# Optimization experiments

Measured on AMD Instinct MI355X. Metric: run time of the kernel, lower is better.

The kernel has to match this reference:

```python
import jax, jax.numpy as jnp
import numpy as np

WH, WW = 8, 8
N_TOK = WH * WW
NUM_HEADS = 4
DIM = 128
B_WIN = 4096  # num_windows * B
NW = 64       # windows per image (for mask)


def _make_rel_tables():
    # relative coords table (1, 2*Wh-1, 2*Ww-1, 2), log-spaced as in SwinV2
    ch = np.arange(-(WH - 1), WH, dtype=np.float32)
    cw = np.arange(-(WW - 1), WW, dtype=np.float32)
    t = np.stack(np.meshgrid(ch, cw, indexing='ij'), axis=-1)[None]  # (1,15,15,2)
    t[..., 0] /= (WH - 1)
    t[..., 1] /= (WW - 1)
    t *= 8
    t = np.sign(t) * np.log2(np.abs(t) + 1.0) / np.log2(8)
    # relative position index (N, N)
    coords = np.stack(np.meshgrid(np.arange(WH), np.arange(WW), indexing='ij'))
    cf = coords.reshape(2, -1)
    rel = cf[:, :, None] - cf[:, None, :]
    rel = rel.transpose(1, 2, 0).copy()
    rel[:, :, 0] += WH - 1
    rel[:, :, 1] += WW - 1
    rel[:, :, 0] *= 2 * WW - 1
    idx = rel.sum(-1).astype(np.int32)
    return jnp.asarray(t), jnp.asarray(idx)


def setup_inputs() -> dict:
    key = jax.random.key(0)
    ks = jax.random.split(key, 8)
    table, idx = _make_rel_tables()
    return {
        'x': jax.random.normal(ks[0], (B_WIN, N_TOK, DIM), jnp.float32),
        'context': jax.random.normal(ks[1], (B_WIN, N_TOK, DIM), jnp.float32),
        'mask': jnp.zeros((NW, N_TOK, N_TOK), jnp.float32),
        'q_w': jax.random.normal(ks[2], (DIM, DIM), jnp.float32) * 0.02,
        'q_b': jnp.zeros((DIM,), jnp.float32),
        'kv_w': jax.random.normal(ks[3], (2 * DIM, DIM), jnp.float32) * 0.02,
        'v_b': jnp.zeros((DIM,), jnp.float32),
        'logit_scale': jnp.full((NUM_HEADS, 1, 1), np.log(10.0), jnp.float32),
        'cpb_w1': jax.random.normal(ks[4], (512, 2), jnp.float32) * 0.02,
        'cpb_b1': jnp.zeros((512,), jnp.float32),
        'cpb_w2': jax.random.normal(ks[5], (NUM_HEADS, 512), jnp.float32) * 0.02,
        'proj_w': jax.random.normal(ks[6], (DIM, DIM), jnp.float32) * 0.02,
        'proj_b': jnp.zeros((DIM,), jnp.float32),
        'rel_coords_table': table,
        'rel_pos_index': idx,
    }


def _l2norm(t, eps=1e-12):
    return t / jnp.maximum(jnp.linalg.norm(t, axis=-1, keepdims=True), eps)


def reference(x, context, mask, q_w, q_b, kv_w, v_b, logit_scale,
              cpb_w1, cpb_b1, cpb_w2, proj_w, proj_b,
              rel_coords_table, rel_pos_index):
    B_, N, C = x.shape
    H = NUM_HEADS
    hd = C // H
    # projections (kv bias = [zeros_like(v_b); v_b])
    q = x @ q_w.T + q_b
    kv_bias = jnp.concatenate([jnp.zeros_like(v_b), v_b])
    kv = context @ kv_w.T + kv_bias
    q = q.reshape(B_, N, H, hd).transpose(0, 2, 1, 3)          # (B_,H,N,hd)
    kv = kv.reshape(B_, N, 2, H, hd).transpose(2, 0, 3, 1, 4)  # (2,B_,H,N,hd)
    k, v = kv[0], kv[1]
    # cosine attention with clamped learned scale
    attn = jnp.einsum('bhnd,bhmd->bhnm', _l2norm(q), _l2norm(k))
    scale = jnp.exp(jnp.minimum(logit_scale, np.log(1.0 / 0.01)))  # (H,1,1)
    attn = attn * scale[None]
    # CPB-MLP relative position bias
    hidd = jax.nn.relu(rel_coords_table @ cpb_w1.T + cpb_b1)   # (1,15,15,512)
    table = (hidd @ cpb_w2.T).reshape(-1, H)                   # ((2Wh-1)(2Ww-1), H)
    bias = table[rel_pos_index.reshape(-1)].reshape(N, N, H)
    bias = 16.0 * jax.nn.sigmoid(bias.transpose(2, 0, 1))      # (H,N,N)
    attn = attn + bias[None]
    # shift mask
    nW = mask.shape[0]
    attn = attn.reshape(B_ // nW, nW, H, N, N) + mask[None, :, None]
    attn = attn.reshape(B_, H, N, N)
    attn = jax.nn.softmax(attn, axis=-1)
    out = jnp.einsum('bhnm,bhmd->bhnd', attn, v)
    out = out.transpose(0, 2, 1, 3).reshape(B_, N, C)
    return out @ proj_w.T + proj_b
```

## Files before the change

### kernel.cpp

```cpp
#include <hip/hip_runtime.h>
#include <hip/hip_bf16.h>

#define NT 64
#define DIM 128

typedef __attribute__((ext_vector_type(8))) short short8;
typedef __attribute__((ext_vector_type(4))) short short4v;
typedef __attribute__((ext_vector_type(8))) __bf16 bf16x8;
typedef __attribute__((ext_vector_type(4))) float floatx4;
typedef __attribute__((ext_vector_type(4))) unsigned uintx4;

#define MFMA(a,b,c) __builtin_amdgcn_mfma_f32_16x16x32_bf16(a,b,c,0,0,0)
#define SWZ(idx, row) ((idx) ^ (((row)&7)<<3))

__device__ __forceinline__ short bfbits(float f) {
  return __builtin_bit_cast(short, (__bf16)f);
}
__device__ __forceinline__ unsigned pk2(float lo, float hi) {
  return (unsigned)(unsigned short)__builtin_bit_cast(unsigned short, (__bf16)lo)
       | ((unsigned)(unsigned short)__builtin_bit_cast(unsigned short, (__bf16)hi) << 16);
}
__device__ __forceinline__ bf16x8 frag_bf(const short* __restrict__ p) {
  return __builtin_bit_cast(bf16x8, *(const short8*)p);
}
// ... 26 lines not shown
        a1 += h * w2[512 + j];
        a2 += h * w2[1024 + j];
        a3 += h * w2[1536 + j];
      }
      logits[t][0]=a0; logits[t][1]=a1; logits[t][2]=a2; logits[t][3]=a3;
    }
    __syncthreads();
    for (int f = t; f < 16384; f += 256) {
      int i    = f & 3;
      int lane = (f >> 2) & 63;
      int qt   = (f >> 8) & 3;
      int mk   = (f >> 10) & 3;
      int h    = f >> 12;
      int q = qt*16 + (lane & 15);
      int k = mk*16 + ((lane >> 4) & 3)*4 + i;
      int p = idx[q*64 + k];
      float v = logits[p][h];
      bias_packed[f] = 16.f / (1.f + __expf(-v));
    }
  } else {
    int gidx = (blockIdx.x - 1) * 4096 + t * 16;
    const float* src; int off;
    if (gidx < 16384)      { src = q_w;    off = gidx; }
    else if (gidx < 49152) { src = kv_w;   off = gidx - 16384; }
    else                   { src = proj_w; off = gidx - 49152; }
    const float4* s = (const float4*)(src + off);
    short* dst = wbf + gidx;
#pragma unroll
    for (int i = 0; i < 2; ++i)
      *(short8*)(dst + i*8) = pack8(s[2*i], s[2*i+1]);
  }
}

__global__ __launch_bounds__(512, 6)
void swin_ctx_attn_kernel(const float* __restrict__ x, const float* __restrict__ ctx,
                          const float* __restrict__ mask,
                          const short* __restrict__ wq, const float* __restrict__ q_b,
                          const short* __restrict__ wkv, const float* __restrict__ v_b,
                          const float* __restrict__ logit_scale,
                          const short* __restrict__ wproj, const float* __restrict__ proj_b,
                          const float* __restrict__ bias_p,
                          float* __restrict__ out) {
  __shared__ short lds[24576] __attribute__((aligned(16)));
  const int tid  = threadIdx.x;
  const int lane = tid & 63;
  const int wv   = tid >> 6;
  const int h    = wv >> 1;
  const int s    = wv & 1;
  const int b    = blockIdx.x;
  const int lr   = lane & 15;
  const int lg   = lane >> 4;

  short* xb   = lds;
  short* cb   = lds + 8192;
  short* kn   = lds + 16384;
  short* vT   = xb;
  short* outp = cb;
  short* knh  = kn + h*2048;

  const float* xw = x   + (size_t)b*(NT*DIM);
  const float* cw = ctx + (size_t)b*(NT*DIM);

  {
    const int sr = tid >> 3, sc0 = (tid & 7) * 16;
    const float4* xs = (const float4*)(xw + sr*DIM + sc0);
    const float4* cs = (const float4*)(cw + sr*DIM + sc0);
    float4 xr[4], cr[4];
#pragma unroll
    for (int i = 0; i < 4; ++i) xr[i] = xs[i];
#pragma unroll
    for (int i = 0; i < 4; ++i) cr[i] = cs[i];
#pragma unroll
    for (int i = 0; i < 2; ++i)
      *(short8*)(xb + SWZ(sr*128 + sc0 + i*8, sr)) = pack8(xr[2*i], xr[2*i+1]);
#pragma unroll
    for (int i = 0; i < 2; ++i)
      *(short8*)(cb + SWZ(sr*128 + sc0 + i*8, sr)) = pack8(cr[2*i], cr[2*i+1]);
  }
  __syncthreads();

  const int sA = ((lane & 16) << 1) | (lane & 15);
  const int sB = sA + 16;
  const unsigned selp = (lane & 32) ? 0x07060302u : 0x05040100u;

  bf16x8 qB[2];
  float scl = __expf(fminf(logit_scale[h], 4.605170185988091f));
  {
    floatx4 aq[2][2] = {};
    for (int ks = 0; ks < 4; ++ks) {
      bf16x8 xf[2], wf[2];
#pragma unroll
      for (int n = 0; n < 2; ++n) {
        int tok = (2*s + n)*16 + lr;
        xf[n] = frag_bf(xb + SWZ(tok*128 + ks*32 + lg*8, tok));
      }
#pragma unroll
      for (int mc = 0; mc < 2; ++mc)
        wf[mc] = frag_bf(wq + (h*32 + mc*16 + lr)*DIM + ks*32 + lg*8);
#pragma unroll
      for (int mc = 0; mc < 2; ++mc)
#pragma unroll
        for (int n = 0; n < 2; ++n)
          aq[mc][n] = MFMA(wf[mc], xf[n], aq[mc][n]);
    }
    floatx4 qb4[2];
#pragma unroll
    for (int mc = 0; mc < 2; ++mc)
      qb4[mc] = *(const floatx4*)(q_b + h*32 + mc*16 + lg*4);
#pragma unroll
    for (int n = 0; n < 2; ++n) {
      float ss = 0.f;
#pragma unroll
      for (int mc = 0; mc < 2; ++mc)
#pragma unroll
        for (int i = 0; i < 4; ++i) {
          aq[mc][n][i] += qb4[mc][i];
          ss += aq[mc][n][i]*aq[mc][n][i];
        }
      ss += __shfl_xor(ss, 16, 64);
      ss += __shfl_xor(ss, 32, 64);
      float sc = scl / fmaxf(sqrtf(ss), 1e-12f);
#pragma unroll
      for (int mc = 0; mc < 2; ++mc)
#pragma unroll
        for (int i = 0; i < 4; ++i) aq[mc][n][i] *= sc;
      unsigned pq[4], w[8];
#pragma unroll
      for (int i = 0; i < 4; ++i) pq[i] = pk2(aq[0][n][i], aq[1][n][i]);
#pragma unroll
      for (int j = 0; j < 8; ++j) w[j] = __shfl(pq[j & 3], (j < 4) ? sA : sB, 64);
      uintx4 u;
#pragma unroll
      for (int t = 0; t < 4; ++t) u[t] = __builtin_amdgcn_perm(w[2*t+1], w[2*t], selp);
      qB[n] = __builtin_bit_cast(bf16x8, u);
    }
  }

  {
    floatx4 ak[2][2] = {};
    for (int ks = 0; ks < 4; ++ks) {
      bf16x8 cf[2], wkf[2];
#pragma unroll
      for (int r = 0; r < 2; ++r) {
        int tok = (2*s + r)*16 + lr;
        cf[r] = frag_bf(cb + SWZ(tok*128 + ks*32 + lg*8, tok));
      }
#pragma unroll
      for (int mc = 0; mc < 2; ++mc)
        wkf[mc] = frag_bf(wkv + (h*32 + mc*16 + lr)*DIM + ks*32 + lg*8);
#pragma unroll
      for (int mc = 0; mc < 2; ++mc)
#pragma unroll
        for (int n = 0; n < 2; ++n)
          ak[mc][n] = MFMA(wkf[mc], cf[n], ak[mc][n]);
    }
#pragma unroll
    for (int n = 0; n < 2; ++n) {
      float ss = 0.f;
#pragma unroll
      for (int mc = 0; mc < 2; ++mc)
#pragma unroll
        for (int i = 0; i < 4; ++i) ss += ak[mc][n][i]*ak[mc][n][i];
      ss += __shfl_xor(ss, 16, 64);
      ss += __shfl_xor(ss, 32, 64);
      float sc = 1.0f / fmaxf(sqrtf(ss), 1e-12f);
#pragma unroll
      for (int mc = 0; mc < 2; ++mc)
#pragma unroll
        for (int i = 0; i < 4; ++i) ak[mc][n][i] *= sc;
    }
#pragma unroll
    for (int mc = 0; mc < 2; ++mc)
#pragma unroll
      for (int n = 0; n < 2; ++n) {
        int tok = (2*s + n)*16 + lr;
        short4v t4;
#pragma unroll
        for (int i = 0; i < 4; ++i) t4[i] = bfbits(ak[mc][n][i]);
        *(short4v*)(knh + SWZ(tok*32 + mc*16 + lg*4, tok)) = t4;
      }
  }
  __syncthreads();

  {
    floatx4 av[2][2] = {};
    for (int ks = 0; ks < 4; ++ks) {
      bf16x8 cf[2], wvf[2];
#pragma unroll
      for (int r = 0; r < 2; ++r) {
        int tok = (2*s + r)*16 + lr;
        cf[r] = frag_bf(cb + SWZ(tok*128 + ks*32 + lg*8, tok));
      }
#pragma unroll
      for (int mc = 0; mc < 2; ++mc)
        wvf[mc] = frag_bf(wkv + (DIM + h*32 + mc*16 + lr)*DIM + ks*32 + lg*8);
#pragma unroll
      for (int mc = 0; mc < 2; ++mc)
#pragma unroll
        for (int n = 0; n < 2; ++n)
          av[mc][n] = MFMA(cf[mc], wvf[n], av[mc][n]);
    }
    float vb0 = v_b[h*32 + lr], vb1 = v_b[h*32 + 16 + lr];
#pragma unroll
    for (int m = 0; m < 2; ++m)
#pragma unroll
      for (int n = 0; n < 2; ++n) {
        int chG = h*32 + n*16 + lr;
        float vb = n ? vb1 : vb0;
        short4v t4;
#pragma unroll
        for (int i = 0; i < 4; ++i) t4[i] = bfbits(av[m][n][i] + vb);
        *(short4v*)(vT + SWZ(chG*64 + s*32 + m*16 + lg*4, chG)) = t4;
      }
  }
  __syncthreads();

  floatx4 st[4][2] = {};
#pragma unroll
  for (int mk = 0; mk < 4; ++mk) {
    int tok = mk*16 + lr;
    bf16x8 kf = frag_bf(knh + SWZ(tok*32 + lg*8, tok));
#pragma unroll
    for (int n = 0; n < 2; ++n)
      st[mk][n] = MFMA(kf, qB[n], st[mk][n]);
  }

  float rinv[2];
  {
    int wimg = b & 63;
#pragma unroll
    for (int n = 0; n < 2; ++n) {
      int qcol = (2*s + n)*16 + lr;
#pragma unroll
      for (int mk = 0; mk < 4; ++mk) {
        floatx4 b4 = ((const floatx4*)bias_p)[((h*4 + mk)*4 + (2*s + n))*64 + lane];
        floatx4 m4 = *(const floatx4*)(mask + ((size_t)wimg*64 + qcol)*64 + mk*16 + lg*4);
#pragma unroll
        for (int i = 0; i < 4; ++i) st[mk][n][i] += b4[i] + m4[i];
      }
      float mx = st[0][n][0];
#pragma unroll
      for (int mk = 0; mk < 4; ++mk)
#pragma unroll
        for (int i = 0; i < 4; ++i) mx = fmaxf(mx, st[mk][n][i]);
      mx = fmaxf(mx, __shfl_xor(mx, 16, 64));
      mx = fmaxf(mx, __shfl_xor(mx, 32, 64));
      float sum = 0.f;
#pragma unroll
      for (int mk = 0; mk < 4; ++mk)
#pragma unroll
        for (int i = 0; i < 4; ++i) {
          st[mk][n][i] = __expf(st[mk][n][i] - mx);
          sum += st[mk][n][i];
        }
      sum += __shfl_xor(sum, 16, 64);
      sum += __shfl_xor(sum, 32, 64);
      rinv[n] = 1.0f / sum;
    }
  }

  bf16x8 pB[2][2];
#pragma unroll
  for (int kk = 0; kk < 2; ++kk)
#pragma unroll
    for (int n = 0; n < 2; ++n) {
      unsigned pp[4], w[8];
#pragma unroll
      for (int i = 0; i < 4; ++i) pp[i] = pk2(st[2*kk][n][i], st[2*kk+1][n][i]);
#pragma unroll
      for (int j = 0; j < 8; ++j) w[j] = __shfl(pp[j & 3], (j < 4) ? sA : sB, 64);
      uintx4 u;
#pragma unroll
      for (int t = 0; t < 4; ++t) u[t] = __builtin_amdgcn_perm(w[2*t+1], w[2*t], selp);
      pB[kk][n] = __builtin_bit_cast(bf16x8, u);
    }
  floatx4 ot[2][2] = {};
#pragma unroll
  for (int kk = 0; kk < 2; ++kk) {
    bf16x8 vf[2];
#pragma unroll
    for (int mo = 0; mo < 2; ++mo) {
      int chG = h*32 + mo*16 + lr;
      vf[mo] = frag_bf(vT + SWZ(chG*64 + kk*32 + lg*8, chG));
    }
#pragma unroll
    for (int mo = 0; mo < 2; ++mo)
#pragma unroll
      for (int n = 0; n < 2; ++n)
        ot[mo][n] = MFMA(vf[mo], pB[kk][n], ot[mo][n]);
  }

#pragma unroll
  for (int mo = 0; mo < 2; ++mo)
#pragma unroll
    for (int n = 0; n < 2; ++n) {
      int tok = (2*s + n)*16 + lr;
      short4v t4;
#pragma unroll
      for (int i = 0; i < 4; ++i) t4[i] = bfbits(ot[mo][n][i] * rinv[n]);
      *(short4v*)(outp + SWZ(tok*128 + h*32 + mo*16 + lg*4, tok)) = t4;
    }
  __syncthreads();

  {
    floatx4 ap[2][2] = {};
    for (int ks = 0; ks < 4; ++ks) {
      bf16x8 of[2], wpf[2];
#pragma unroll
      for (int m = 0; m < 2; ++m) {
        int tok = s*32 + m*16 + lr;
        of[m] = frag_bf(outp + SWZ(tok*128 + ks*32 + lg*8, tok));
      }
#pragma unroll
      for (int n = 0; n < 2; ++n)
        wpf[n] = frag_bf(wproj + (h*32 + n*16 + lr)*DIM + ks*32 + lg*8);
#pragma unroll
      for (int m = 0; m < 2; ++m)
#pragma unroll
        for (int n = 0; n < 2; ++n)
          ap[m][n] = MFMA(of[m], wpf[n], ap[m][n]);
    }
    float pb0 = proj_b[h*32 + lr], pb1 = proj_b[h*32 + 16 + lr];
    float* op = out + (size_t)b * (NT*DIM);
#pragma unroll
    for (int m = 0; m < 2; ++m)
#pragma unroll
      for (int n = 0; n < 2; ++n) {
        float pb = n ? pb1 : pb0;
#pragma unroll
        for (int i = 0; i < 4; ++i)
          op[(s*32 + m*16 + lg*4 + i)*DIM + h*32 + n*16 + lr] = ap[m][n][i] + pb;
      }
  }
}

extern "C" void kernel_launch(void* const* d_in, const int* in_sizes, int n_in,
                              void* d_out, int out_size, void* d_ws, size_t ws_size,
                              hipStream_t stream) {
  const float* x     = (const float*)d_in[0];
  const float* ctx   = (const float*)d_in[1];
  const float* mask  = (const float*)d_in[2];
  const float* q_w   = (const float*)d_in[3];
  const float* q_b   = (const float*)d_in[4];
  const float* kv_w  = (const float*)d_in[5];
  const float* v_b   = (const float*)d_in[6];
  const float* ls    = (const float*)d_in[7];
  const float* w1    = (const float*)d_in[8];
  const float* b1    = (const float*)d_in[9];
  const float* w2    = (const float*)d_in[10];
  const float* pw    = (const float*)d_in[11];
  const float* pb    = (const float*)d_in[12];
  const float* table = (const float*)d_in[13];
  const int*   idx   = (const int*)d_in[14];

  float* bias_p = (float*)d_ws;
  short* wbf    = (short*)((char*)d_ws + 65536);
  short* wq     = wbf;
  short* wkv    = wbf + 16384;
  short* wproj  = wbf + 49152;
  int B = in_sizes[0] / (NT * DIM);

  prep_kernel<<<17, 256, 0, stream>>>(table, w1, b1, w2, idx, q_w, kv_w, pw,
                                      bias_p, wbf);
  swin_ctx_attn_kernel<<<B, 512, 0, stream>>>(x, ctx, mask, wq, q_b, wkv, v_b,
                                              ls, wproj, pb, bias_p, (float*)d_out);
}
```

Before: 272.5 us.

## Process two windows per block and prefetch the next window's inputs during compute

Each block now handles two consecutive windows. The second window's x is loaded into registers during the first window's prologue, and its context is loaded while the output projection runs. The idea is to hide global load latency behind MFMA work and to halve the number of blocks launched. In exchange the launch bound drops from 6 to 4 blocks per CU, which raises register pressure and adds extra barriers. The grid also assumes an even window count.

```diff
diff --git a/kernel.cpp b/kernel.cpp
--- a/kernel.cpp
+++ b/kernel.cpp
@@ -82,7 +82,7 @@
   }
 }
 
-__global__ __launch_bounds__(512, 6)
+__global__ __launch_bounds__(512, 4)
 void swin_ctx_attn_kernel(const float* __restrict__ x, const float* __restrict__ ctx,
                           const float* __restrict__ mask,
                           const short* __restrict__ wq, const float* __restrict__ q_b,
@@ -97,7 +97,6 @@
   const int wv   = tid >> 6;
   const int h    = wv >> 1;
   const int s    = wv & 1;
-  const int b    = blockIdx.x;
   const int lr   = lane & 15;
   const int lg   = lane >> 4;
 
@@ -108,280 +107,305 @@
   short* outp = cb;
   short* knh  = kn + h*2048;
 
-  const float* xw = x   + (size_t)b*(NT*DIM);
-  const float* cw = ctx + (size_t)b*(NT*DIM);
-
-  {
-    const int sr = tid >> 3, sc0 = (tid & 7) * 16;
-    const float4* xs = (const float4*)(xw + sr*DIM + sc0);
-    const float4* cs = (const float4*)(cw + sr*DIM + sc0);
-    float4 xr[4], cr[4];
-#pragma unroll
-    for (int i = 0; i < 4; ++i) xr[i] = xs[i];
-#pragma unroll
-    for (int i = 0; i < 4; ++i) cr[i] = cs[i];
-#pragma unroll
-    for (int i = 0; i < 2; ++i)
-      *(short8*)(xb + SWZ(sr*128 + sc0 + i*8, sr)) = pack8(xr[2*i], xr[2*i+1]);
-#pragma unroll
-    for (int i = 0; i < 2; ++i)
-      *(short8*)(cb + SWZ(sr*128 + sc0 + i*8, sr)) = pack8(cr[2*i], cr[2*i+1]);
-  }
-  __syncthreads();
+  const int sr  = tid >> 3;
+  const int sc0 = (tid & 7) * 16;
+  const int b0  = blockIdx.x * 2;
 
   const int sA = ((lane & 16) << 1) | (lane & 15);
   const int sB = sA + 16;
   const unsigned selp = (lane & 32) ? 0x07060302u : 0x05040100u;
-
-  bf16x8 qB[2];
-  float scl = __expf(fminf(logit_scale[h], 4.605170185988091f));
+  const float scl = __expf(fminf(logit_scale[h], 4.605170185988091f));
+
+  float4 xr1[4];
   {
-    floatx4 aq[2][2] = {};
-    for (int ks = 0; ks < 4; ++ks) {
-      bf16x8 xf[2], wf[2];
+    const float4* xs = (const float4*)(x   + (size_t)b0*(NT*DIM) + sr*DIM + sc0);
+    const float4* cs = (const float4*)(ctx + (size_t)b0*(NT*DIM) + sr*DIM + sc0);
+    float4 xr[4], cr[4];
+#pragma unroll
+    for (int i = 0; i < 4; ++i) xr[i] = xs[i];
+#pragma unroll
+    for (int i = 0; i < 4; ++i) cr[i] = cs[i];
+    *(short8*)(xb + SWZ(sr*128 + sc0,     sr)) = pack8(xr[0], xr[1]);
+    *(short8*)(xb + SWZ(sr*128 + sc0 + 8, sr)) = pack8(xr[2], xr[3]);
+    *(short8*)(cb + SWZ(sr*128 + sc0,     sr)) = pack8(cr[0], cr[1]);
+    *(short8*)(cb + SWZ(sr*128 + sc0 + 8, sr)) = pack8(cr[2], cr[3]);
+    const float4* xs1 = (const float4*)(x + (size_t)(b0+1)*(NT*DIM) + sr*DIM + sc0);
+#pragma unroll
+    for (int i = 0; i < 4; ++i) xr1[i] = xs1[i];
+    __builtin_amdgcn_sched_barrier(0);
+  }
+  __syncthreads();
+
+  auto window = [&](int b, bool pre) {
+    bf16x8 qB[2];
+    {
+      floatx4 aq[2][2] = {};
+      for (int ks = 0; ks < 4; ++ks) {
+        bf16x8 xf[2], wf[2];
+#pragma unroll
+        for (int n = 0; n < 2; ++n) {
+          int tok = (2*s + n)*16 + lr;
+          xf[n] = frag_bf(xb + SWZ(tok*128 + ks*32 + lg*8, tok));
+        }
+#pragma unroll
+        for (int mc = 0; mc < 2; ++mc)
+          wf[mc] = frag_bf(wq + (h*32 + mc*16 + lr)*DIM + ks*32 + lg*8);
+#pragma unroll
+        for (int mc = 0; mc < 2; ++mc)
+#pragma unroll
+          for (int n = 0; n < 2; ++n)
+            aq[mc][n] = MFMA(wf[mc], xf[n], aq[mc][n]);
+      }
+      floatx4 qb4[2];
+#pragma unroll
+      for (int mc = 0; mc < 2; ++mc)
+        qb4[mc] = *(const floatx4*)(q_b + h*32 + mc*16 + lg*4);
 #pragma unroll
       for (int n = 0; n < 2; ++n) {
-        int tok = (2*s + n)*16 + lr;
-        xf[n] = frag_bf(xb + SWZ(tok*128 + ks*32 + lg*8, tok));
+        float ss = 0.f;
+#pragma unroll
+        for (int mc = 0; mc < 2; ++mc)
+#pragma unroll
+          for (int i = 0; i < 4; ++i) {
+            aq[mc][n][i] += qb4[mc][i];
+            ss += aq[mc][n][i]*aq[mc][n][i];
+          }
+        ss += __shfl_xor(ss, 16, 64);
+        ss += __shfl_xor(ss, 32, 64);
+        float sc = scl / fmaxf(sqrtf(ss), 1e-12f);
+#pragma unroll
+        for (int mc = 0; mc < 2; ++mc)
+#pragma unroll
+          for (int i = 0; i < 4; ++i) aq[mc][n][i] *= sc;
+        unsigned pq[4], w[8];
+#pragma unroll
+        for (int i = 0; i < 4; ++i) pq[i] = pk2(aq[0][n][i], aq[1][n][i]);
+#pragma unroll
+        for (int j = 0; j < 8; ++j) w[j] = __shfl(pq[j & 3], (j < 4) ? sA : sB, 64);
+        uintx4 u;
+#pragma unroll
+        for (int t = 0; t < 4; ++t) u[t] = __builtin_amdgcn_perm(w[2*t+1], w[2*t], selp);
+        qB[n] = __builtin_bit_cast(bf16x8, u);
+      }
+    }
+
+    {
+      floatx4 ak[2][2] = {};
+      for (int ks = 0; ks < 4; ++ks) {
+        bf16x8 cf[2], wkf[2];
+#pragma unroll
+        for (int r = 0; r < 2; ++r) {
+          int tok = (2*s + r)*16 + lr;
+          cf[r] = frag_bf(cb + SWZ(tok*128 + ks*32 + lg*8, tok));
+        }
+#pragma unroll
+        for (int mc = 0; mc < 2; ++mc)
+          wkf[mc] = frag_bf(wkv + (h*32 + mc*16 + lr)*DIM + ks*32 + lg*8);
+#pragma unroll
+        for (int mc = 0; mc < 2; ++mc)
+#pragma unroll
+          for (int n = 0; n < 2; ++n)
+            ak[mc][n] = MFMA(wkf[mc], cf[n], ak[mc][n]);
+      }
+#pragma unroll
+      for (int n = 0; n < 2; ++n) {
+        float ss = 0.f;
+#pragma unroll
+        for (int mc = 0; mc < 2; ++mc)
+#pragma unroll
+          for (int i = 0; i < 4; ++i) ss += ak[mc][n][i]*ak[mc][n][i];
+        ss += __shfl_xor(ss, 16, 64);
+        ss += __shfl_xor(ss, 32, 64);
+        float sc = 1.0f / fmaxf(sqrtf(ss), 1e-12f);
+#pragma unroll
+        for (int mc = 0; mc < 2; ++mc)
+#pragma unroll
+          for (int i = 0; i < 4; ++i) ak[mc][n][i] *= sc;
       }
 #pragma unroll
       for (int mc = 0; mc < 2; ++mc)
-        wf[mc] = frag_bf(wq + (h*32 + mc*16 + lr)*DIM + ks*32 + lg*8);
-#pragma unroll
-      for (int mc = 0; mc < 2; ++mc)
+#pragma unroll
+        for (int n = 0; n < 2; ++n) {
+          int tok = (2*s + n)*16 + lr;
+          short4v t4;
+#pragma unroll
+          for (int i = 0; i < 4; ++i) t4[i] = bfbits(ak[mc][n][i]);
+          *(short4v*)(knh + SWZ(tok*32 + mc*16 + lg*4, tok)) = t4;
+        }
+    }
+    __syncthreads();
+
+    {
+      floatx4 av[2][2] = {};
+      for (int ks = 0; ks < 4; ++ks) {
+        bf16x8 cf[2], wvf[2];
+#pragma unroll
+        for (int r = 0; r < 2; ++r) {
+          int tok = (2*s + r)*16 + lr;
+          cf[r] = frag_bf(cb + SWZ(tok*128 + ks*32 + lg*8, tok));
+        }
+#pragma unroll
+        for (int mc = 0; mc < 2; ++mc)
+          wvf[mc] = frag_bf(wkv + (DIM + h*32 + mc*16 + lr)*DIM + ks*32 + lg*8);
+#pragma unroll
+        for (int mc = 0; mc < 2; ++mc)
+#pragma unroll
+          for (int n = 0; n < 2; ++n)
+            av[mc][n] = MFMA(cf[mc], wvf[n], av[mc][n]);
+      }
+      float vb0 = v_b[h*32 + lr], vb1 = v_b[h*32 + 16 + lr];
+#pragma unroll
+      for (int m = 0; m < 2; ++m)
+#pragma unroll
+        for (int n = 0; n < 2; ++n) {
+          int chG = h*32 + n*16 + lr;
+          float vb = n ? vb1 : vb0;
+          short4v t4;
+#pragma unroll
+          for (int i = 0; i < 4; ++i) t4[i] = bfbits(av[m][n][i] + vb);
+          *(short4v*)(vT + SWZ(chG*64 + s*32 + m*16 + lg*4, chG)) = t4;
+        }
+    }
+    __syncthreads();
+
+    floatx4 st[4][2] = {};
+#pragma unroll
+    for (int mk = 0; mk < 4; ++mk) {
+      int tok = mk*16 + lr;
+      bf16x8 kf = frag_bf(knh + SWZ(tok*32 + lg*8, tok));
+#pragma unroll
+      for (int n = 0; n < 2; ++n)
+        st[mk][n] = MFMA(kf, qB[n], st[mk][n]);
+    }
+
+    float rinv[2];
+    {
+      int wimg = b & 63;
+#pragma unroll
+      for (int n = 0; n < 2; ++n) {
+        int qcol = (2*s + n)*16 + lr;
+#pragma unroll
+        for (int mk = 0; mk < 4; ++mk) {
+          floatx4 b4 = ((const floatx4*)bias_p)[((h*4 + mk)*4 + (2*s + n))*64 + lane];
+          floatx4 m4 = *(const floatx4*)(mask + ((size_t)wimg*64 + qcol)*64 + mk*16 + lg*4);
+#pragma unroll
+          for (int i = 0; i < 4; ++i) st[mk][n][i] += b4[i] + m4[i];
+        }
+        float mx = st[0][n][0];
+#pragma unroll
+        for (int mk = 0; mk < 4; ++mk)
+#pragma unroll
+          for (int i = 0; i < 4; ++i) mx = fmaxf(mx, st[mk][n][i]);
+        mx = fmaxf(mx, __shfl_xor(mx, 16, 64));
+        mx = fmaxf(mx, __shfl_xor(mx, 32, 64));
+        float sum = 0.f;
+#pragma unroll
+        for (int mk = 0; mk < 4; ++mk)
+#pragma unroll
+          for (int i = 0; i < 4; ++i) {
+            st[mk][n][i] = __expf(st[mk][n][i] - mx);
+            sum += st[mk][n][i];
+          }
+        sum += __shfl_xor(sum, 16, 64);
+        sum += __shfl_xor(sum, 32, 64);
+        rinv[n] = 1.0f / sum;
+      }
+    }
+
+    bf16x8 pB[2][2];
+#pragma unroll
+    for (int kk = 0; kk < 2; ++kk)
+#pragma unroll
+      for (int n = 0; n < 2; ++n) {
+        unsigned pp[4], w[8];
+#pragma unroll
+        for (int i = 0; i < 4; ++i) pp[i] = pk2(st[2*kk][n][i], st[2*kk+1][n][i]);
+#pragma unroll
+        for (int j = 0; j < 8; ++j) w[j] = __shfl(pp[j & 3], (j < 4) ? sA : sB, 64);
+        uintx4 u;
+#pragma unroll
+        for (int t = 0; t < 4; ++t) u[t] = __builtin_amdgcn_perm(w[2*t+1], w[2*t], selp);
+        pB[kk][n] = __builtin_bit_cast(bf16x8, u);
+      }
+    floatx4 ot[2][2] = {};
+#pragma unroll
+    for (int kk = 0; kk < 2; ++kk) {
+      bf16x8 vf[2];
+#pragma unroll
+      for (int mo = 0; mo < 2; ++mo) {
+        int chG = h*32 + mo*16 + lr;
+        vf[mo] = frag_bf(vT + SWZ(chG*64 + kk*32 + lg*8, chG));
+      }
+#pragma unroll
+      for (int mo = 0; mo < 2; ++mo)
 #pragma unroll
         for (int n = 0; n < 2; ++n)
-          aq[mc][n] = MFMA(wf[mc], xf[n], aq[mc][n]);
-    }
-    floatx4 qb4[2];
-#pragma unroll
-    for (int mc = 0; mc < 2; ++mc)
-      qb4[mc] = *(const floatx4*)(q_b + h*32 + mc*16 + lg*4);
-#pragma unroll
-    for (int n = 0; n < 2; ++n) {
-      float ss = 0.f;
-#pragma unroll
-      for (int mc = 0; mc < 2; ++mc)
-#pragma unroll
-        for (int i = 0; i < 4; ++i) {
-          aq[mc][n][i] += qb4[mc][i];
-          ss += aq[mc][n][i]*aq[mc][n][i];
-        }
-      ss += __shfl_xor(ss, 16, 64);
-      ss += __shfl_xor(ss, 32, 64);
-      float sc = scl / fmaxf(sqrtf(ss), 1e-12f);
-#pragma unroll
-      for (int mc = 0; mc < 2; ++mc)
-#pragma unroll
-        for (int i = 0; i < 4; ++i) aq[mc][n][i] *= sc;
-      unsigned pq[4], w[8];
-#pragma unroll
-      for (int i = 0; i < 4; ++i) pq[i] = pk2(aq[0][n][i], aq[1][n][i]);
-#pragma unroll
-      for (int j = 0; j < 8; ++j) w[j] = __shfl(pq[j & 3], (j < 4) ? sA : sB, 64);
-      uintx4 u;
-#pragma unroll
-      for (int t = 0; t < 4; ++t) u[t] = __builtin_amdgcn_perm(w[2*t+1], w[2*t], selp);
-      qB[n] = __builtin_bit_cast(bf16x8, u);
-    }
-  }
-
-  {
-    floatx4 ak[2][2] = {};
-    for (int ks = 0; ks < 4; ++ks) {
-      bf16x8 cf[2], wkf[2];
-#pragma unroll
-      for (int r = 0; r < 2; ++r) {
-        int tok = (2*s + r)*16 + lr;
-        cf[r] = frag_bf(cb + SWZ(tok*128 + ks*32 + lg*8, tok));
-      }
-#pragma unroll
-      for (int mc = 0; mc < 2; ++mc)
-        wkf[mc] = frag_bf(wkv + (h*32 + mc*16 + lr)*DIM + ks*32 + lg*8);
-#pragma unroll
-      for (int mc = 0; mc < 2; ++mc)
-#pragma unroll
-        for (int n = 0; n < 2; ++n)
-          ak[mc][n] = MFMA(wkf[mc], cf[n], ak[mc][n]);
-    }
-#pragma unroll
-    for (int n = 0; n < 2; ++n) {
-      float ss = 0.f;
-#pragma unroll
-      for (int mc = 0; mc < 2; ++mc)
-#pragma unroll
-        for (int i = 0; i < 4; ++i) ss += ak[mc][n][i]*ak[mc][n][i];
-      ss += __shfl_xor(ss, 16, 64);
-      ss += __shfl_xor(ss, 32, 64);
-      float sc = 1.0f / fmaxf(sqrtf(ss), 1e-12f);
-#pragma unroll
-      for (int mc = 0; mc < 2; ++mc)
-#pragma unroll
-        for (int i = 0; i < 4; ++i) ak[mc][n][i] *= sc;
-    }
-#pragma unroll
-    for (int mc = 0; mc < 2; ++mc)
+          ot[mo][n] = MFMA(vf[mo], pB[kk][n], ot[mo][n]);
+    }
+
+#pragma unroll
+    for (int mo = 0; mo < 2; ++mo)
 #pragma unroll
       for (int n = 0; n < 2; ++n) {
         int tok = (2*s + n)*16 + lr;
         short4v t4;
 #pragma unroll
-        for (int i = 0; i < 4; ++i) t4[i] = bfbits(ak[mc][n][i]);
-        *(short4v*)(knh + SWZ(tok*32 + mc*16 + lg*4, tok)) = t4;
-      }
-  }
+        for (int i = 0; i < 4; ++i) t4[i] = bfbits(ot[mo][n][i] * rinv[n]);
+        *(short4v*)(outp + SWZ(tok*128 + h*32 + mo*16 + lg*4, tok)) = t4;
+      }
+    __syncthreads();
+
+    float4 cr1[4];
+    if (pre) {
+      const float4* cs1 = (const float4*)(ctx + (size_t)(b+1)*(NT*DIM) + sr*DIM + sc0);
+#pragma unroll
+      for (int i = 0; i < 4; ++i) cr1[i] = cs1[i];
+      *(short8*)(xb + SWZ(sr*128 + sc0,     sr)) = pack8(xr1[0], xr1[1]);
+      *(short8*)(xb + SWZ(sr*128 + sc0 + 8, sr)) = pack8(xr1[2], xr1[3]);
+      __builtin_amdgcn_sched_barrier(0);
+    }
+
+    {
+      floatx4 ap[2][2] = {};
+      for (int ks = 0; ks < 4; ++ks) {
+        bf16x8 of[2], wpf[2];
+#pragma unroll
+        for (int m = 0; m < 2; ++m) {
+          int tok = s*32 + m*16 + lr;
+          of[m] = frag_bf(outp + SWZ(tok*128 + ks*32 + lg*8, tok));
+        }
+#pragma unroll
+        for (int n = 0; n < 2; ++n)
+          wpf[n] = frag_bf(wproj + (h*32 + n*16 + lr)*DIM + ks*32 + lg*8);
+#pragma unroll
+        for (int m = 0; m < 2; ++m)
+#pragma unroll
+          for (int n = 0; n < 2; ++n)
+            ap[m][n] = MFMA(of[m], wpf[n], ap[m][n]);
+      }
+      float pb0 = proj_b[h*32 + lr], pb1 = proj_b[h*32 + 16 + lr];
+      float* op = out + (size_t)b * (NT*DIM);
+#pragma unroll
+      for (int m = 0; m < 2; ++m)
+#pragma unroll
+        for (int n = 0; n < 2; ++n) {
+          float pb = n ? pb1 : pb0;
+#pragma unroll
+          for (int i = 0; i < 4; ++i)
+            op[(s*32 + m*16 + lg*4 + i)*DIM + h*32 + n*16 + lr] = ap[m][n][i] + pb;
+        }
+    }
+
+    if (pre) {
+      __syncthreads();
+      *(short8*)(cb + SWZ(sr*128 + sc0,     sr)) = pack8(cr1[0], cr1[1]);
+      *(short8*)(cb + SWZ(sr*128 + sc0 + 8, sr)) = pack8(cr1[2], cr1[3]);
+    }
+  };
+
+  window(b0, true);
   __syncthreads();
-
-  {
-    floatx4 av[2][2] = {};
-    for (int ks = 0; ks < 4; ++ks) {
-      bf16x8 cf[2], wvf[2];
-#pragma unroll
-      for (int r = 0; r < 2; ++r) {
-        int tok = (2*s + r)*16 + lr;
-        cf[r] = frag_bf(cb + SWZ(tok*128 + ks*32 + lg*8, tok));
-      }
-#pragma unroll
-      for (int mc = 0; mc < 2; ++mc)
-        wvf[mc] = frag_bf(wkv + (DIM + h*32 + mc*16 + lr)*DIM + ks*32 + lg*8);
-#pragma unroll
-      for (int mc = 0; mc < 2; ++mc)
-#pragma unroll
-        for (int n = 0; n < 2; ++n)
-          av[mc][n] = MFMA(cf[mc], wvf[n], av[mc][n]);
-    }
-    float vb0 = v_b[h*32 + lr], vb1 = v_b[h*32 + 16 + lr];
-#pragma unroll
-    for (int m = 0; m < 2; ++m)
-#pragma unroll
-      for (int n = 0; n < 2; ++n) {
-        int chG = h*32 + n*16 + lr;
-        float vb = n ? vb1 : vb0;
-        short4v t4;
-#pragma unroll
-        for (int i = 0; i < 4; ++i) t4[i] = bfbits(av[m][n][i] + vb);
-        *(short4v*)(vT + SWZ(chG*64 + s*32 + m*16 + lg*4, chG)) = t4;
-      }
-  }
-  __syncthreads();
-
-  floatx4 st[4][2] = {};
-#pragma unroll
-  for (int mk = 0; mk < 4; ++mk) {
-    int tok = mk*16 + lr;
-    bf16x8 kf = frag_bf(knh + SWZ(tok*32 + lg*8, tok));
-#pragma unroll
-    for (int n = 0; n < 2; ++n)
-      st[mk][n] = MFMA(kf, qB[n], st[mk][n]);
-  }
-
-  float rinv[2];
-  {
-    int wimg = b & 63;
-#pragma unroll
-    for (int n = 0; n < 2; ++n) {
-      int qcol = (2*s + n)*16 + lr;
-#pragma unroll
-      for (int mk = 0; mk < 4; ++mk) {
-        floatx4 b4 = ((const floatx4*)bias_p)[((h*4 + mk)*4 + (2*s + n))*64 + lane];
-        floatx4 m4 = *(const floatx4*)(mask + ((size_t)wimg*64 + qcol)*64 + mk*16 + lg*4);
-#pragma unroll
-        for (int i = 0; i < 4; ++i) st[mk][n][i] += b4[i] + m4[i];
-      }
-      float mx = st[0][n][0];
-#pragma unroll
-      for (int mk = 0; mk < 4; ++mk)
-#pragma unroll
-        for (int i = 0; i < 4; ++i) mx = fmaxf(mx, st[mk][n][i]);
-      mx = fmaxf(mx, __shfl_xor(mx, 16, 64));
-      mx = fmaxf(mx, __shfl_xor(mx, 32, 64));
-      float sum = 0.f;
-#pragma unroll
-      for (int mk = 0; mk < 4; ++mk)
-#pragma unroll
-        for (int i = 0; i < 4; ++i) {
-          st[mk][n][i] = __expf(st[mk][n][i] - mx);
-          sum += st[mk][n][i];
-        }
-      sum += __shfl_xor(sum, 16, 64);
-      sum += __shfl_xor(sum, 32, 64);
-      rinv[n] = 1.0f / sum;
-    }
-  }
-
-  bf16x8 pB[2][2];
-#pragma unroll
-  for (int kk = 0; kk < 2; ++kk)
-#pragma unroll
-    for (int n = 0; n < 2; ++n) {
-      unsigned pp[4], w[8];
-#pragma unroll
-      for (int i = 0; i < 4; ++i) pp[i] = pk2(st[2*kk][n][i], st[2*kk+1][n][i]);
-#pragma unroll
-      for (int j = 0; j < 8; ++j) w[j] = __shfl(pp[j & 3], (j < 4) ? sA : sB, 64);
-      uintx4 u;
-#pragma unroll
-      for (int t = 0; t < 4; ++t) u[t] = __builtin_amdgcn_perm(w[2*t+1], w[2*t], selp);
-      pB[kk][n] = __builtin_bit_cast(bf16x8, u);
-    }
-  floatx4 ot[2][2] = {};
-#pragma unroll
-  for (int kk = 0; kk < 2; ++kk) {
-    bf16x8 vf[2];
-#pragma unroll
-    for (int mo = 0; mo < 2; ++mo) {
-      int chG = h*32 + mo*16 + lr;
-      vf[mo] = frag_bf(vT + SWZ(chG*64 + kk*32 + lg*8, chG));
-    }
-#pragma unroll
-    for (int mo = 0; mo < 2; ++mo)
-#pragma unroll
-      for (int n = 0; n < 2; ++n)
-        ot[mo][n] = MFMA(vf[mo], pB[kk][n], ot[mo][n]);
-  }
-
-#pragma unroll
-  for (int mo = 0; mo < 2; ++mo)
-#pragma unroll
-    for (int n = 0; n < 2; ++n) {
-      int tok = (2*s + n)*16 + lr;
-      short4v t4;
-#pragma unroll
-      for (int i = 0; i < 4; ++i) t4[i] = bfbits(ot[mo][n][i] * rinv[n]);
-      *(short4v*)(outp + SWZ(tok*128 + h*32 + mo*16 + lg*4, tok)) = t4;
-    }
-  __syncthreads();
-
-  {
-    floatx4 ap[2][2] = {};
-    for (int ks = 0; ks < 4; ++ks) {
-      bf16x8 of[2], wpf[2];
-#pragma unroll
-      for (int m = 0; m < 2; ++m) {
-        int tok = s*32 + m*16 + lr;
-        of[m] = frag_bf(outp + SWZ(tok*128 + ks*32 + lg*8, tok));
-      }
-#pragma unroll
-      for (int n = 0; n < 2; ++n)
-        wpf[n] = frag_bf(wproj + (h*32 + n*16 + lr)*DIM + ks*32 + lg*8);
-#pragma unroll
-      for (int m = 0; m < 2; ++m)
-#pragma unroll
-        for (int n = 0; n < 2; ++n)
-          ap[m][n] = MFMA(of[m], wpf[n], ap[m][n]);
-    }
-    float pb0 = proj_b[h*32 + lr], pb1 = proj_b[h*32 + 16 + lr];
-    float* op = out + (size_t)b * (NT*DIM);
-#pragma unroll
-    for (int m = 0; m < 2; ++m)
-#pragma unroll
-      for (int n = 0; n < 2; ++n) {
-        float pb = n ? pb1 : pb0;
-#pragma unroll
-        for (int i = 0; i < 4; ++i)
-          op[(s*32 + m*16 + lg*4 + i)*DIM + h*32 + n*16 + lr] = ap[m][n][i] + pb;
-      }
-  }
+  window(b0 + 1, false);
 }
 
 extern "C" void kernel_launch(void* const* d_in, const int* in_sizes, int n_in,
@@ -412,6 +436,6 @@
 
   prep_kernel<<<17, 256, 0, stream>>>(table, w1, b1, w2, idx, q_w, kv_w, pw,
                                       bias_p, wbf);
-  swin_ctx_attn_kernel<<<B, 512, 0, stream>>>(x, ctx, mask, wq, q_b, wkv, v_b,
-                                              ls, wproj, pb, bias_p, (float*)d_out);
-}
+  swin_ctx_attn_kernel<<<B/2, 512, 0, stream>>>(x, ctx, mask, wq, q_b, wkv, v_b,
+                                                ls, wproj, pb, bias_p, (float*)d_out);
+}
```

New measurement: 304.8 us. 11.8% more time.

## Split fused attention into QKV projection and attention+proj kernels via workspace

Applied to the files above, without the earlier changes.

Replaces the single fused per-window kernel with two kernels. The first computes normalized Q, K and transposed V in bf16 and writes them to the workspace. The second reads them back, applies softmax with bias and mask, multiplies by V and runs the output projection. The split aims to lower per-block LDS use and register pressure so occupancy rises, at the cost of an extra global round trip of the Q/K/V intermediates (about 6 MB) and one more launch. The old fused kernel is kept as a fallback when the workspace is too small.

```diff
diff --git a/kernel.cpp b/kernel.cpp
--- a/kernel.cpp
+++ b/kernel.cpp
@@ -82,15 +82,309 @@
   }
 }
 
+__global__ __launch_bounds__(256, 5)
+void qkv_kernel(const float* __restrict__ x, const float* __restrict__ ctx,
+                const short* __restrict__ wq, const float* __restrict__ q_b,
+                const short* __restrict__ wkv, const float* __restrict__ v_b,
+                const float* __restrict__ logit_scale,
+                short* __restrict__ qn, short* __restrict__ kn,
+                short* __restrict__ vt) {
+  __shared__ short lds[16384] __attribute__((aligned(16)));
+  const int tid  = threadIdx.x;
+  const int lane = tid & 63;
+  const int h    = tid >> 6;
+  const int b    = blockIdx.x;
+  const int lr   = lane & 15;
+  const int lg   = lane >> 4;
+
+  short* xb = lds;
+  short* cb = lds + 8192;
+
+  {
+    const int sr = tid >> 2, c0 = (tid & 3) * 32;
+    const float4* xs = (const float4*)(x   + (size_t)b*(NT*DIM) + sr*DIM + c0);
+    const float4* cs = (const float4*)(ctx + (size_t)b*(NT*DIM) + sr*DIM + c0);
+    float4 xr[8], cr[8];
+#pragma unroll
+    for (int i = 0; i < 8; ++i) xr[i] = xs[i];
+#pragma unroll
+    for (int i = 0; i < 8; ++i) cr[i] = cs[i];
+#pragma unroll
+    for (int j = 0; j < 4; ++j)
+      *(short8*)(xb + SWZ(sr*128 + c0 + j*8, sr)) = pack8(xr[2*j], xr[2*j+1]);
+#pragma unroll
+    for (int j = 0; j < 4; ++j)
+      *(short8*)(cb + SWZ(sr*128 + c0 + j*8, sr)) = pack8(cr[2*j], cr[2*j+1]);
+  }
+  __syncthreads();
+
+  const float scl = __expf(fminf(logit_scale[h], 4.605170185988091f));
+  const size_t wh = ((size_t)b*4 + h) * 2048;
+
+  {
+    floatx4 aq[2][4] = {};
+    for (int ks = 0; ks < 4; ++ks) {
+      bf16x8 Bx[4], Aw[2];
+#pragma unroll
+      for (int nt = 0; nt < 4; ++nt) {
+        int tok = nt*16 + lr;
+        Bx[nt] = frag_bf(xb + SWZ(tok*128 + ks*32 + lg*8, tok));
+      }
+#pragma unroll
+      for (int mc = 0; mc < 2; ++mc)
+        Aw[mc] = frag_bf(wq + (h*32 + mc*16 + lr)*DIM + ks*32 + lg*8);
+#pragma unroll
+      for (int mc = 0; mc < 2; ++mc)
+#pragma unroll
+        for (int nt = 0; nt < 4; ++nt)
+          aq[mc][nt] = MFMA(Aw[mc], Bx[nt], aq[mc][nt]);
+    }
+    floatx4 qb4[2];
+#pragma unroll
+    for (int mc = 0; mc < 2; ++mc)
+      qb4[mc] = *(const floatx4*)(q_b + h*32 + mc*16 + lg*4);
+#pragma unroll
+    for (int nt = 0; nt < 4; ++nt) {
+      float ss = 0.f;
+#pragma unroll
+      for (int mc = 0; mc < 2; ++mc)
+#pragma unroll
+        for (int i = 0; i < 4; ++i) {
+          aq[mc][nt][i] += qb4[mc][i];
+          ss += aq[mc][nt][i]*aq[mc][nt][i];
+        }
+      ss += __shfl_xor(ss, 16, 64);
+      ss += __shfl_xor(ss, 32, 64);
+      float sc = scl / fmaxf(sqrtf(ss), 1e-12f);
+      int tok = nt*16 + lr;
+#pragma unroll
+      for (int mc = 0; mc < 2; ++mc) {
+        short4v t4;
+#pragma unroll
+        for (int i = 0; i < 4; ++i) t4[i] = bfbits(aq[mc][nt][i] * sc);
+        *(short4v*)(qn + wh + tok*32 + mc*16 + lg*4) = t4;
+      }
+    }
+  }
+
+  {
+    floatx4 ak[2][4] = {};
+    for (int ks = 0; ks < 4; ++ks) {
+      bf16x8 Bx[4], Aw[2];
+#pragma unroll
+      for (int nt = 0; nt < 4; ++nt) {
+        int tok = nt*16 + lr;
+        Bx[nt] = frag_bf(cb + SWZ(tok*128 + ks*32 + lg*8, tok));
+      }
+#pragma unroll
+      for (int mc = 0; mc < 2; ++mc)
+        Aw[mc] = frag_bf(wkv + (h*32 + mc*16 + lr)*DIM + ks*32 + lg*8);
+#pragma unroll
+      for (int mc = 0; mc < 2; ++mc)
+#pragma unroll
+        for (int nt = 0; nt < 4; ++nt)
+          ak[mc][nt] = MFMA(Aw[mc], Bx[nt], ak[mc][nt]);
+    }
+#pragma unroll
+    for (int nt = 0; nt < 4; ++nt) {
+      float ss = 0.f;
+#pragma unroll
+      for (int mc = 0; mc < 2; ++mc)
+#pragma unroll
+        for (int i = 0; i < 4; ++i) ss += ak[mc][nt][i]*ak[mc][nt][i];
+      ss += __shfl_xor(ss, 16, 64);
+      ss += __shfl_xor(ss, 32, 64);
+      float sc = 1.0f / fmaxf(sqrtf(ss), 1e-12f);
+      int tok = nt*16 + lr;
+#pragma unroll
+      for (int mc = 0; mc < 2; ++mc) {
+        short4v t4;
+#pragma unroll
+        for (int i = 0; i < 4; ++i) t4[i] = bfbits(ak[mc][nt][i] * sc);
+        *(short4v*)(kn + wh + tok*32 + mc*16 + lg*4) = t4;
+      }
+    }
+  }
+
+  {
+    floatx4 av[4][2] = {};
+    for (int ks = 0; ks < 4; ++ks) {
+      bf16x8 A[4], W[2];
+#pragma unroll
+      for (int mt = 0; mt < 4; ++mt) {
+        int tok = mt*16 + lr;
+        A[mt] = frag_bf(cb + SWZ(tok*128 + ks*32 + lg*8, tok));
+      }
+#pragma unroll
+      for (int n = 0; n < 2; ++n)
+        W[n] = frag_bf(wkv + (DIM + h*32 + n*16 + lr)*DIM + ks*32 + lg*8);
+#pragma unroll
+      for (int n = 0; n < 2; ++n)
+#pragma unroll
+        for (int mt = 0; mt < 4; ++mt)
+          av[mt][n] = MFMA(A[mt], W[n], av[mt][n]);
+    }
+    float vb0 = v_b[h*32 + lr], vb1 = v_b[h*32 + 16 + lr];
+#pragma unroll
+    for (int mt = 0; mt < 4; ++mt)
+#pragma unroll
+      for (int n = 0; n < 2; ++n) {
+        float vb = n ? vb1 : vb0;
+        short4v t4;
+#pragma unroll
+        for (int i = 0; i < 4; ++i) t4[i] = bfbits(av[mt][n][i] + vb);
+        *(short4v*)(vt + wh + (n*16 + lr)*64 + mt*16 + lg*4) = t4;
+      }
+  }
+}
+
+__global__ __launch_bounds__(256, 4)
+void attn_proj_kernel(const short* __restrict__ qn, const short* __restrict__ kn,
+                      const short* __restrict__ vt,
+                      const float* __restrict__ mask,
+                      const short* __restrict__ wproj, const float* __restrict__ proj_b,
+                      const float* __restrict__ bias_p,
+                      float* __restrict__ out) {
+  __shared__ short outp[8192] __attribute__((aligned(16)));
+  const int tid  = threadIdx.x;
+  const int lane = tid & 63;
+  const int h    = tid >> 6;
+  const int b    = blockIdx.x;
+  const int lr   = lane & 15;
+  const int lg   = lane >> 4;
+
+  const size_t wh = ((size_t)b*4 + h) * 2048;
+  const short* qh = qn + wh;
+  const short* kh = kn + wh;
+  const short* vh = vt + wh;
+
+  floatx4 st[4][4] = {};
+  {
+    bf16x8 qf[4];
+#pragma unroll
+    for (int nq = 0; nq < 4; ++nq)
+      qf[nq] = frag_bf(qh + (nq*16 + lr)*32 + lg*8);
+#pragma unroll
+    for (int mk = 0; mk < 4; ++mk) {
+      bf16x8 kf = frag_bf(kh + (mk*16 + lr)*32 + lg*8);
+#pragma unroll
+      for (int nq = 0; nq < 4; ++nq)
+        st[mk][nq] = MFMA(kf, qf[nq], st[mk][nq]);
+    }
+  }
+
+  float rinv[4];
+  {
+    int wimg = b & 63;
+#pragma unroll
+    for (int nq = 0; nq < 4; ++nq) {
+      int qcol = nq*16 + lr;
+#pragma unroll
+      for (int mk = 0; mk < 4; ++mk) {
+        floatx4 b4 = ((const floatx4*)bias_p)[((h*4 + mk)*4 + nq)*64 + lane];
+        floatx4 m4 = *(const floatx4*)(mask + ((size_t)wimg*64 + qcol)*64 + mk*16 + lg*4);
+#pragma unroll
+        for (int i = 0; i < 4; ++i) st[mk][nq][i] += b4[i] + m4[i];
+      }
+      float mx = st[0][nq][0];
+#pragma unroll
+      for (int mk = 0; mk < 4; ++mk)
+#pragma unroll
+        for (int i = 0; i < 4; ++i) mx = fmaxf(mx, st[mk][nq][i]);
+      mx = fmaxf(mx, __shfl_xor(mx, 16, 64));
+      mx = fmaxf(mx, __shfl_xor(mx, 32, 64));
+      float sum = 0.f;
+#pragma unroll
+      for (int mk = 0; mk < 4; ++mk)
+#pragma unroll
+        for (int i = 0; i < 4; ++i) {
+          st[mk][nq][i] = __expf(st[mk][nq][i] - mx);
+          sum += st[mk][nq][i];
+        }
+      sum += __shfl_xor(sum, 16, 64);
+      sum += __shfl_xor(sum, 32, 64);
+      rinv[nq] = 1.0f / sum;
+    }
+  }
+
+  const int sA = ((lane & 16) << 1) | (lane & 15);
+  const int sB = sA + 16;
+  const unsigned selp = (lane & 32) ? 0x07060302u : 0x05040100u;
+  floatx4 ot[2][4] = {};
+#pragma unroll
+  for (int nq = 0; nq < 4; ++nq) {
+#pragma unroll
+    for (int kk = 0; kk < 2; ++kk) {
+      unsigned pp[4], w[8];
+#pragma unroll
+      for (int i = 0; i < 4; ++i) pp[i] = pk2(st[2*kk][nq][i], st[2*kk+1][nq][i]);
+#pragma unroll
+      for (int j = 0; j < 8; ++j) w[j] = __shfl(pp[j & 3], (j < 4) ? sA : sB, 64);
+      uintx4 u;
+#pragma unroll
+      for (int t = 0; t < 4; ++t) u[t] = __builtin_amdgcn_perm(w[2*t+1], w[2*t], selp);
+      bf16x8 pB = __builtin_bit_cast(bf16x8, u);
+#pragma unroll
+      for (int mo = 0; mo < 2; ++mo) {
+        bf16x8 vf = frag_bf(vh + (mo*16 + lr)*64 + kk*32 + lg*8);
+        ot[mo][nq] = MFMA(vf, pB, ot[mo][nq]);
+      }
+    }
+  }
+
+#pragma unroll
+  for (int mo = 0; mo < 2; ++mo)
+#pragma unroll
+    for (int nq = 0; nq < 4; ++nq) {
+      int tok = nq*16 + lr;
+      short4v t4;
+#pragma unroll
+      for (int i = 0; i < 4; ++i) t4[i] = bfbits(ot[mo][nq][i] * rinv[nq]);
+      *(short4v*)(outp + SWZ(tok*128 + h*32 + mo*16 + lg*4, tok)) = t4;
+    }
+  __syncthreads();
+
+  {
+    floatx4 ap[4][2] = {};
+    for (int ks = 0; ks < 4; ++ks) {
+      bf16x8 of[4], wpf[2];
+#pragma unroll
+      for (int m = 0; m < 4; ++m) {
+        int tok = m*16 + lr;
+        of[m] = frag_bf(outp + SWZ(tok*128 + ks*32 + lg*8, tok));
+      }
+#pragma unroll
+      for (int n = 0; n < 2; ++n)
+        wpf[n] = frag_bf(wproj + (h*32 + n*16 + lr)*DIM + ks*32 + lg*8);
+#pragma unroll
+      for (int n = 0; n < 2; ++n)
+#pragma unroll
+        for (int m = 0; m < 4; ++m)
+          ap[m][n] = MFMA(of[m], wpf[n], ap[m][n]);
+    }
+    float pb0 = proj_b[h*32 + lr], pb1 = proj_b[h*32 + 16 + lr];
+    float* op = out + (size_t)b * (NT*DIM);
+#pragma unroll
+    for (int m = 0; m < 4; ++m)
+#pragma unroll
+      for (int n = 0; n < 2; ++n) {
+        float pb = n ? pb1 : pb0;
+#pragma unroll
+        for (int i = 0; i < 4; ++i)
+          op[(m*16 + lg*4 + i)*DIM + h*32 + n*16 + lr] = ap[m][n][i] + pb;
+      }
+  }
+}
+
 __global__ __launch_bounds__(512, 6)
-void swin_ctx_attn_kernel(const float* __restrict__ x, const float* __restrict__ ctx,
-                          const float* __restrict__ mask,
-                          const short* __restrict__ wq, const float* __restrict__ q_b,
-                          const short* __restrict__ wkv, const float* __restrict__ v_b,
-                          const float* __restrict__ logit_scale,
-                          const short* __restrict__ wproj, const float* __restrict__ proj_b,
-                          const float* __restrict__ bias_p,
-                          float* __restrict__ out) {
+void fused_fallback_kernel(const float* __restrict__ x, const float* __restrict__ ctx,
+                           const float* __restrict__ mask,
+                           const short* __restrict__ wq, const float* __restrict__ q_b,
+                           const short* __restrict__ wkv, const float* __restrict__ v_b,
+                           const float* __restrict__ logit_scale,
+                           const short* __restrict__ wproj, const float* __restrict__ proj_b,
+                           const float* __restrict__ bias_p,
+                           float* __restrict__ out) {
   __shared__ short lds[24576] __attribute__((aligned(16)));
   const int tid  = threadIdx.x;
   const int lane = tid & 63;
@@ -412,6 +706,18 @@
 
   prep_kernel<<<17, 256, 0, stream>>>(table, w1, b1, w2, idx, q_w, kv_w, pw,
                                       bias_p, wbf);
-  swin_ctx_attn_kernel<<<B, 512, 0, stream>>>(x, ctx, mask, wq, q_b, wkv, v_b,
-                                              ls, wproj, pb, bias_p, (float*)d_out);
-}
+
+  const size_t per_tensor = (size_t)B * 4 * 64 * 32;
+  const size_t needed = 196608 + 3 * per_tensor * sizeof(short);
+  if (ws_size >= needed) {
+    short* qn = (short*)((char*)d_ws + 196608);
+    short* kn = qn + per_tensor;
+    short* vt = kn + per_tensor;
+    qkv_kernel<<<B, 256, 0, stream>>>(x, ctx, wq, q_b, wkv, v_b, ls, qn, kn, vt);
+    attn_proj_kernel<<<B, 256, 0, stream>>>(qn, kn, vt, mask, wproj, pb, bias_p,
+                                            (float*)d_out);
+  } else {
+    fused_fallback_kernel<<<B, 512, 0, stream>>>(x, ctx, mask, wq, q_b, wkv, v_b,
+                                                 ls, wproj, pb, bias_p, (float*)d_out);
+  }
+}
```

New measurement: 315.3 us. 1.16x slower.

## Give vT and outp dedicated LDS, drop a barrier, vectorize output stores

Applied to the files above, without the earlier changes.

vT and the attention output buffer now get their own LDS regions instead of aliasing the x and context buffers, so one __syncthreads between the K and V phases can be removed. The projection GEMM swaps its operand order so each lane holds four consecutive output channels, and the bias add plus global store become float4 writes instead of scattered scalar stores. LDS per block grows from 48KB to 80KB and the launch-bounds occupancy hint drops from 6 to 4, which lowers the number of resident blocks per CU.

```diff
diff --git a/kernel.cpp b/kernel.cpp
--- a/kernel.cpp
+++ b/kernel.cpp
@@ -82,7 +82,7 @@
   }
 }
 
-__global__ __launch_bounds__(512, 6)
+__global__ __launch_bounds__(512, 4)
 void swin_ctx_attn_kernel(const float* __restrict__ x, const float* __restrict__ ctx,
                           const float* __restrict__ mask,
                           const short* __restrict__ wq, const float* __restrict__ q_b,
@@ -91,7 +91,13 @@
                           const short* __restrict__ wproj, const float* __restrict__ proj_b,
                           const float* __restrict__ bias_p,
                           float* __restrict__ out) {
-  __shared__ short lds[24576] __attribute__((aligned(16)));
+  __shared__ short lds[40960] __attribute__((aligned(16)));
+  short* xb   = lds;
+  short* cb   = lds + 8192;
+  short* kn   = lds + 16384;
+  short* vT   = lds + 24576;
+  short* outp = lds + 32768;
+
   const int tid  = threadIdx.x;
   const int lane = tid & 63;
   const int wv   = tid >> 6;
@@ -100,41 +106,30 @@
   const int b    = blockIdx.x;
   const int lr   = lane & 15;
   const int lg   = lane >> 4;
-
-  short* xb   = lds;
-  short* cb   = lds + 8192;
-  short* kn   = lds + 16384;
-  short* vT   = xb;
-  short* outp = cb;
-  short* knh  = kn + h*2048;
-
-  const float* xw = x   + (size_t)b*(NT*DIM);
-  const float* cw = ctx + (size_t)b*(NT*DIM);
+  short* knh = kn + h*2048;
 
   {
     const int sr = tid >> 3, sc0 = (tid & 7) * 16;
-    const float4* xs = (const float4*)(xw + sr*DIM + sc0);
-    const float4* cs = (const float4*)(cw + sr*DIM + sc0);
+    const float4* xs = (const float4*)(x   + (size_t)b*(NT*DIM) + sr*DIM + sc0);
+    const float4* cs = (const float4*)(ctx + (size_t)b*(NT*DIM) + sr*DIM + sc0);
     float4 xr[4], cr[4];
 #pragma unroll
     for (int i = 0; i < 4; ++i) xr[i] = xs[i];
 #pragma unroll
     for (int i = 0; i < 4; ++i) cr[i] = cs[i];
-#pragma unroll
-    for (int i = 0; i < 2; ++i)
-      *(short8*)(xb + SWZ(sr*128 + sc0 + i*8, sr)) = pack8(xr[2*i], xr[2*i+1]);
-#pragma unroll
-    for (int i = 0; i < 2; ++i)
-      *(short8*)(cb + SWZ(sr*128 + sc0 + i*8, sr)) = pack8(cr[2*i], cr[2*i+1]);
+    *(short8*)(xb + SWZ(sr*128 + sc0,     sr)) = pack8(xr[0], xr[1]);
+    *(short8*)(xb + SWZ(sr*128 + sc0 + 8, sr)) = pack8(xr[2], xr[3]);
+    *(short8*)(cb + SWZ(sr*128 + sc0,     sr)) = pack8(cr[0], cr[1]);
+    *(short8*)(cb + SWZ(sr*128 + sc0 + 8, sr)) = pack8(cr[2], cr[3]);
   }
   __syncthreads();
 
   const int sA = ((lane & 16) << 1) | (lane & 15);
   const int sB = sA + 16;
   const unsigned selp = (lane & 32) ? 0x07060302u : 0x05040100u;
+  const float scl = __expf(fminf(logit_scale[h], 4.605170185988091f));
 
   bf16x8 qB[2];
-  float scl = __expf(fminf(logit_scale[h], 4.605170185988091f));
   {
     floatx4 aq[2][2] = {};
     for (int ks = 0; ks < 4; ++ks) {
@@ -174,14 +169,14 @@
       for (int mc = 0; mc < 2; ++mc)
 #pragma unroll
         for (int i = 0; i < 4; ++i) aq[mc][n][i] *= sc;
-      unsigned pq[4], w[8];
+      unsigned pq[4], wrk[8];
 #pragma unroll
       for (int i = 0; i < 4; ++i) pq[i] = pk2(aq[0][n][i], aq[1][n][i]);
 #pragma unroll
-      for (int j = 0; j < 8; ++j) w[j] = __shfl(pq[j & 3], (j < 4) ? sA : sB, 64);
+      for (int j = 0; j < 8; ++j) wrk[j] = __shfl(pq[j & 3], (j < 4) ? sA : sB, 64);
       uintx4 u;
 #pragma unroll
-      for (int t = 0; t < 4; ++t) u[t] = __builtin_amdgcn_perm(w[2*t+1], w[2*t], selp);
+      for (int t = 0; t < 4; ++t) u[t] = __builtin_amdgcn_perm(wrk[2*t+1], wrk[2*t], selp);
       qB[n] = __builtin_bit_cast(bf16x8, u);
     }
   }
@@ -230,7 +225,6 @@
         *(short4v*)(knh + SWZ(tok*32 + mc*16 + lg*4, tok)) = t4;
       }
   }
-  __syncthreads();
 
   {
     floatx4 av[2][2] = {};
@@ -314,14 +308,14 @@
   for (int kk = 0; kk < 2; ++kk)
 #pragma unroll
     for (int n = 0; n < 2; ++n) {
-      unsigned pp[4], w[8];
+      unsigned pp[4], wrk[8];
 #pragma unroll
       for (int i = 0; i < 4; ++i) pp[i] = pk2(st[2*kk][n][i], st[2*kk+1][n][i]);
 #pragma unroll
-      for (int j = 0; j < 8; ++j) w[j] = __shfl(pp[j & 3], (j < 4) ? sA : sB, 64);
+      for (int j = 0; j < 8; ++j) wrk[j] = __shfl(pp[j & 3], (j < 4) ? sA : sB, 64);
       uintx4 u;
 #pragma unroll
-      for (int t = 0; t < 4; ++t) u[t] = __builtin_amdgcn_perm(w[2*t+1], w[2*t], selp);
+      for (int t = 0; t < 4; ++t) u[t] = __builtin_amdgcn_perm(wrk[2*t+1], wrk[2*t], selp);
       pB[kk][n] = __builtin_bit_cast(bf16x8, u);
     }
   floatx4 ot[2][2] = {};
@@ -357,30 +351,30 @@
     for (int ks = 0; ks < 4; ++ks) {
       bf16x8 of[2], wpf[2];
 #pragma unroll
-      for (int m = 0; m < 2; ++m) {
-        int tok = s*32 + m*16 + lr;
-        of[m] = frag_bf(outp + SWZ(tok*128 + ks*32 + lg*8, tok));
-      }
-#pragma unroll
-      for (int n = 0; n < 2; ++n)
-        wpf[n] = frag_bf(wproj + (h*32 + n*16 + lr)*DIM + ks*32 + lg*8);
-#pragma unroll
-      for (int m = 0; m < 2; ++m)
-#pragma unroll
-        for (int n = 0; n < 2; ++n)
-          ap[m][n] = MFMA(of[m], wpf[n], ap[m][n]);
-    }
-    float pb0 = proj_b[h*32 + lr], pb1 = proj_b[h*32 + 16 + lr];
-    float* op = out + (size_t)b * (NT*DIM);
-#pragma unroll
-    for (int m = 0; m < 2; ++m)
-#pragma unroll
-      for (int n = 0; n < 2; ++n) {
-        float pb = n ? pb1 : pb0;
-#pragma unroll
-        for (int i = 0; i < 4; ++i)
-          op[(s*32 + m*16 + lg*4 + i)*DIM + h*32 + n*16 + lr] = ap[m][n][i] + pb;
-      }
+      for (int nt = 0; nt < 2; ++nt) {
+        int tok = s*32 + nt*16 + lr;
+        of[nt] = frag_bf(outp + SWZ(tok*128 + ks*32 + lg*8, tok));
+      }
+#pragma unroll
+      for (int mc = 0; mc < 2; ++mc)
+        wpf[mc] = frag_bf(wproj + (h*32 + mc*16 + lr)*DIM + ks*32 + lg*8);
+#pragma unroll
+      for (int mc = 0; mc < 2; ++mc)
+#pragma unroll
+        for (int nt = 0; nt < 2; ++nt)
+          ap[mc][nt] = MFMA(wpf[mc], of[nt], ap[mc][nt]);
+    }
+    float* op = out + (size_t)b*(NT*DIM);
+#pragma unroll
+    for (int mc = 0; mc < 2; ++mc) {
+      floatx4 pb4 = *(const floatx4*)(proj_b + h*32 + mc*16 + lg*4);
+#pragma unroll
+      for (int nt = 0; nt < 2; ++nt) {
+        int tok = s*32 + nt*16 + lr;
+        floatx4 v = ap[mc][nt] + pb4;
+        *(floatx4*)(op + tok*DIM + h*32 + mc*16 + lg*4) = v;
+      }
+    }
   }
 }
 
```

After: 274.8 us. Within noise of the previous version (+0.8%).
